# Kernel tuning notes

Measured on AMD Instinct MI355X. Metric: run time of the kernel, lower is better.

## Reference

```python
import jax, jax.numpy as jnp
import numpy as np

N, E, IN_DIM, H, D = 40000, 640000, 128, 8, 16


def setup_inputs() -> dict:
    key = jax.random.key(0)
    k_h, k_s, k_d, k_q, k_k, k_v = jax.random.split(key, 6)
    scale = float(np.sqrt(2.0 / (IN_DIM + H * D)))  # xavier-ish
    return {
        "h": jax.random.normal(k_h, (N, IN_DIM), dtype=jnp.float32),
        "src": jax.random.randint(k_s, (E,), 0, N, dtype=jnp.int32),
        "dst": jax.random.randint(k_d, (E,), 0, N, dtype=jnp.int32),
        "WQ": jax.random.normal(k_q, (IN_DIM, H * D), dtype=jnp.float32) * scale,
        "WK": jax.random.normal(k_k, (IN_DIM, H * D), dtype=jnp.float32) * scale,
        "WV": jax.random.normal(k_v, (IN_DIM, H * D), dtype=jnp.float32) * scale,
    }


def reference(h, src, dst, WQ, WK, WV):
    n = h.shape[0]
    Q = (h @ WQ).reshape(n, H, D)  # [N,H,D]
    K = (h @ WK).reshape(n, H, D)
    V = (h @ WV).reshape(n, H, D)
    inv_sqrt_d = 1.0 / jnp.sqrt(jnp.asarray(D, dtype=h.dtype))
    # per-edge elementwise score (DGL u_mul_v keeps the H x D vector)
    score = K[src] * Q[dst] * inv_sqrt_d  # [E,H,D]
    wV = jax.ops.segment_sum(V[src] * score, dst, num_segments=n)  # [N,H,D]
    z = jax.ops.segment_sum(score, dst, num_segments=n)            # [N,H,D]
    return wV / (z + 1e-6)
```

## Files before the change

kernel.cpp:

```cpp
#include <hip/hip_runtime.h>


#define FMA4(acc, s, b) do { \
    (acc).x = fmaf((s), (b).x, (acc).x); \
    (acc).y = fmaf((s), (b).y, (acc).y); \
    (acc).z = fmaf((s), (b).z, (acc).z); \
    (acc).w = fmaf((s), (b).w, (acc).w); } while (0)

__global__ __launch_bounds__(256) void gemm_qkv(
    const float* __restrict__ h,
    const float* __restrict__ WQ,
    const float* __restrict__ WK,
    const float* __restrict__ WV,
    float* __restrict__ Qf,
    float* __restrict__ KV,
    int N)
{
    __shared__ float4 Wl[32 * 32];
    __shared__ float4 Hl[128 * 8];
    const int t = threadIdx.x;
    const int which = blockIdx.y;
    const float* Wsel = (which == 0) ? WQ : ((which == 1) ? WK : WV);
    const float4* W4 = (const float4*)Wsel;
    const int r0 = blockIdx.x * 128;

    const int tc = t & 15;
    const int tr = t >> 4;

    float4 acc[8][2];
#pragma unroll
    for (int i = 0; i < 8; ++i) {
        acc[i][0] = make_float4(0.f, 0.f, 0.f, 0.f);
        acc[i][1] = make_float4(0.f, 0.f, 0.f, 0.f);
    }

    for (int kc = 0; kc < 4; ++kc) {
        __syncthreads();
#pragma unroll
        for (int i = 0; i < 4; ++i) {
            const int idx = t + i * 256;
            const int k = idx >> 5, c = idx & 31;
            Wl[idx] = W4[(size_t)(kc * 32 + k) * 32 + c];
        }
#pragma unroll
        for (int i = 0; i < 4; ++i) {
            const int idx = t + i * 256;
            const int row = idx >> 3, kk = idx & 7;
            float4 v = make_float4(0.f, 0.f, 0.f, 0.f);
            if (r0 + row < N)
                v = ((const float4*)h)[(size_t)(r0 + row) * 32 + kc * 8 + kk];
            Hl[row * 8 + kk] = v;
        }
        __syncthreads();

        for (int k4 = 0; k4 < 8; ++k4) {
            const float4 b0a = Wl[(k4 * 4 + 0) * 32 + tc * 2];
            const float4 b0b = Wl[(k4 * 4 + 0) * 32 + tc * 2 + 1];
            const float4 b1a = Wl[(k4 * 4 + 1) * 32 + tc * 2];
            const float4 b1b = Wl[(k4 * 4 + 1) * 32 + tc * 2 + 1];
            const float4 b2a = Wl[(k4 * 4 + 2) * 32 + tc * 2];
            const float4 b2b = Wl[(k4 * 4 + 2) * 32 + tc * 2 + 1];
            const float4 b3a = Wl[(k4 * 4 + 3) * 32 + tc * 2];
            const float4 b3b = Wl[(k4 * 4 + 3) * 32 + tc * 2 + 1];
#pragma unroll
            for (int r = 0; r < 8; ++r) {
                const float4 a = Hl[(tr * 8 + r) * 8 + k4];
                FMA4(acc[r][0], a.x, b0a); FMA4(acc[r][1], a.x, b0b);
                FMA4(acc[r][0], a.y, b1a); FMA4(acc[r][1], a.y, b1b);
                FMA4(acc[r][0], a.z, b2a); FMA4(acc[r][1], a.z, b2b);
                FMA4(acc[r][0], a.w, b3a); FMA4(acc[r][1], a.w, b3b);
            }
        }
    }

    float4* Obase = (which == 0) ? (float4*)Qf : (float4*)KV;
    const int ostride = (which == 0) ? 32 : 64;
    const int ooff = (which == 2) ? 32 : 0;
#pragma unroll
    for (int r = 0; r < 8; ++r) {
        const int row = r0 + tr * 8 + r;
        if (row < N) {
            Obase[(size_t)row * ostride + ooff + tc * 2]     = acc[r][0];
            Obase[(size_t)row * ostride + ooff + tc * 2 + 1] = acc[r][1];
        }
    }
}

__global__ __launch_bounds__(256) void count_deg(
    const int* __restrict__ dst, int* __restrict__ deg, int E)
{
    const int e = blockIdx.x * 256 + threadIdx.x;
    if (e < E) atomicAdd(&deg[dst[e]], 1);
}

__global__ __launch_bounds__(256) void chunk_reduce(
    const int* __restrict__ deg, int* __restrict__ csum, int N)
{
    const int t = threadIdx.x;
    const int i = blockIdx.x * 256 + t;
    int x = (i < N) ? deg[i] : 0;
#pragma unroll
    for (int off = 32; off; off >>= 1) x += __shfl_down(x, off, 64);
    __shared__ int ws[4];
    if ((t & 63) == 0) ws[t >> 6] = x;
    __syncthreads();
    if (t == 0) csum[blockIdx.x] = ws[0] + ws[1] + ws[2] + ws[3];
}

__global__ __launch_bounds__(256) void scan_chunks(
    const int* __restrict__ csum, int* __restrict__ coff, int nChunks)
{
    __shared__ int s[256];
    __shared__ int carry;
    const int t = threadIdx.x;
    if (t == 0) carry = 0;
    __syncthreads();
    for (int base = 0; base < nChunks; base += 256) {
        const int i = base + t;
        int x = (i < nChunks) ? csum[i] : 0;
        s[t] = x;
        __syncthreads();
        for (int off = 1; off < 256; off <<= 1) {
            int v = (t >= off) ? s[t - off] : 0;
            __syncthreads();
            s[t] += v;
            __syncthreads();
        }
        if (i < nChunks) coff[i] = carry + s[t] - x;
        __syncthreads();
        if (t == 0) carry += s[255];
        __syncthreads();
    }
}

__global__ __launch_bounds__(256) void chunk_scan(
    const int* __restrict__ deg, const int* __restrict__ coff,
    int* __restrict__ rowptr, int N)
{
    __shared__ int s[256];
    const int t = threadIdx.x;
    const int i = blockIdx.x * 256 + t;
    int x = (i < N) ? deg[i] : 0;
    s[t] = x;
    __syncthreads();
    for (int off = 1; off < 256; off <<= 1) {
        int v = (t >= off) ? s[t - off] : 0;
        __syncthreads();
        s[t] += v;
        __syncthreads();
    }
    if (i < N) rowptr[i + 1] = coff[blockIdx.x] + s[t];
    if (i == 0) rowptr[0] = 0;
}

__global__ __launch_bounds__(256) void scatter_pairs(
    const int* __restrict__ dst, const int* __restrict__ src,
    const int* __restrict__ rowptr, int* __restrict__ cur,
    int2* __restrict__ pairs, int E)
{
    const int e = blockIdx.x * 256 + threadIdx.x;
    if (e >= E) return;
    const int d = dst[e];
    const int pos = rowptr[d] + atomicAdd(&cur[d], 1);
    pairs[pos] = make_int2(e, src[e]);
}

__global__ __launch_bounds__(256) void rank_emit(
    const int* __restrict__ rowptr, const int2* __restrict__ pairs,
    int* __restrict__ srcs, int N)
{
    const int wave = threadIdx.x >> 6;
    const int lane = threadIdx.x & 63;
    const int d = blockIdx.x * 4 + wave;
    if (d >= N) return;
    const int lo = rowptr[d];
    const int deg = rowptr[d + 1] - lo;
    if (deg <= 64) {
        int2 p = make_int2(0x7fffffff, 0);
        if (lane < deg) p = pairs[lo + lane];
        int rank = 0;
        for (int j = 0; j < deg; ++j) {
            const int kj = __shfl(p.x, j, 64);
            rank += (kj < p.x) ? 1 : 0;
        }
        if (lane < deg) srcs[lo + rank] = p.y;
    } else if (lane == 0) {
        for (int i = 0; i < deg; ++i) {
            const int2 pi = pairs[lo + i];
            int rank = 0;
            for (int j = 0; j < deg; ++j) rank += (pairs[lo + j].x < pi.x) ? 1 : 0;
            srcs[lo + rank] = pi.y;
        }
    }
}

__global__ __launch_bounds__(128) void attn_out(
    const int* __restrict__ srcs, const int* __restrict__ rowptr,
    const float* __restrict__ KV, const float* __restrict__ Qf,
    float* __restrict__ out, int N)
{
#pragma clang fp contract(off)
    const int wave = threadIdx.x >> 6;
    const int lane = threadIdx.x & 63;
    const int d = blockIdx.x * 2 + wave;
    if (d >= N) return;
    const float2 q = ((const float2*)Qf)[(size_t)d * 64 + lane];
    const int lo = rowptr[d], hi = rowptr[d + 1];
    const float2* KV2 = (const float2*)KV;
    float2 z = make_float2(0.f, 0.f), wv = z;

#define EDGE_UPD(k, v) do { \
        float sc0 = ((k).x * q.x) * 0.25f; z.x = z.x + sc0; wv.x = wv.x + (v).x * sc0; \
        float sc1 = ((k).y * q.y) * 0.25f; z.y = z.y + sc1; wv.y = wv.y + (v).y * sc1; \
    } while (0)

    int i = lo;
    for (; i + 8 <= hi; i += 8) {
        int s[8];
#pragma unroll
        for (int u = 0; u < 8; ++u) s[u] = srcs[i + u];
        float2 kk[8], vv[8];
#pragma unroll
        for (int u = 0; u < 8; ++u) {
            kk[u] = KV2[(size_t)s[u] * 128 + lane];
            vv[u] = KV2[(size_t)s[u] * 128 + 64 + lane];
        }
#pragma unroll
        for (int u = 0; u < 8; ++u) EDGE_UPD(kk[u], vv[u]);
    }
    for (; i + 4 <= hi; i += 4) {
        const int s0 = srcs[i + 0], s1 = srcs[i + 1];
        const int s2 = srcs[i + 2], s3 = srcs[i + 3];
        const float2 k0 = KV2[(size_t)s0 * 128 + lane], v0 = KV2[(size_t)s0 * 128 + 64 + lane];
        const float2 k1 = KV2[(size_t)s1 * 128 + lane], v1 = KV2[(size_t)s1 * 128 + 64 + lane];
        const float2 k2 = KV2[(size_t)s2 * 128 + lane], v2 = KV2[(size_t)s2 * 128 + 64 + lane];
        const float2 k3 = KV2[(size_t)s3 * 128 + lane], v3 = KV2[(size_t)s3 * 128 + 64 + lane];
        EDGE_UPD(k0, v0); EDGE_UPD(k1, v1); EDGE_UPD(k2, v2); EDGE_UPD(k3, v3);
    }
    for (; i < hi; ++i) {
        const int s = srcs[i];
        const float2 k = KV2[(size_t)s * 128 + lane], v = KV2[(size_t)s * 128 + 64 + lane];
        EDGE_UPD(k, v);
    }
#undef EDGE_UPD

    float2 o;
    o.x = wv.x / (z.x + 1e-6f);
    o.y = wv.y / (z.y + 1e-6f);
    ((float2*)out)[(size_t)d * 64 + lane] = o;
}

extern "C" void kernel_launch(void* const* d_in, const int* in_sizes, int n_in,
                              void* d_out, int out_size, void* d_ws, size_t ws_size,
                              hipStream_t stream)
{
    const float* h  = (const float*)d_in[0];
    const int* src  = (const int*)d_in[1];
    const int* dst  = (const int*)d_in[2];
    const float* WQ = (const float*)d_in[3];
    const float* WK = (const float*)d_in[4];
    const float* WV = (const float*)d_in[5];
    const int N = in_sizes[0] / 128;
    const int E = in_sizes[1];
    const size_t NC = (size_t)N * 128;
    const int nChunks = (N + 255) / 256;

    float* KV = (float*)d_ws;
    float* Qf = KV + (size_t)N * 256;
    int* deg    = (int*)(Qf + NC);
    int* cur    = deg + N;
    int* rowptr = cur + N;
    int* csum   = rowptr + (N + 2);
    int* coff   = csum + nChunks;
    int* srcs   = coff + nChunks;
    int2* pairs = (int2*)(srcs + E);
    float* outp = (float*)d_out;

    hipMemsetAsync(deg, 0, (size_t)2 * N * sizeof(int), stream);

    dim3 ggrid((N + 127) / 128, 3);
    gemm_qkv<<<ggrid, 256, 0, stream>>>(h, WQ, WK, WV, Qf, KV, N);

    const int eb = (E + 255) / 256;
    count_deg<<<eb, 256, 0, stream>>>(dst, deg, E);
    chunk_reduce<<<nChunks, 256, 0, stream>>>(deg, csum, N);
    scan_chunks<<<1, 256, 0, stream>>>(csum, coff, nChunks);
    chunk_scan<<<nChunks, 256, 0, stream>>>(deg, coff, rowptr, N);
    scatter_pairs<<<eb, 256, 0, stream>>>(dst, src, rowptr, cur, pairs, E);
    rank_emit<<<(N + 3) / 4, 256, 0, stream>>>(rowptr, pairs, srcs, N);

    attn_out<<<(N + 1) / 2, 128, 0, stream>>>(srcs, rowptr, KV, Qf, outp, N);
}
```

Baseline: 302.1 us.

## Swizzle GEMM LDS, scatter edge ids only, prefetch next source indices

The QKV GEMM now stores h tiles in LDS with an XOR swizzle and spreads each thread's output columns as tc and tc+16, aiming to cut LDS bank conflicts. The CSR build scatters plain edge ids instead of (edge, src) pairs, halving that scatter's traffic, and looks up src[e] during the rank step. The attention kernel software-pipelines its 8-edge loop so the next batch of source indices loads while the current K/V gathers are consumed. This adds a dependent random read of src in rank_emit and more register pressure in attn_out.

```diff
diff --git a/kernel.cpp b/kernel.cpp
--- a/kernel.cpp
+++ b/kernel.cpp
@@ -49,22 +49,23 @@
             float4 v = make_float4(0.f, 0.f, 0.f, 0.f);
             if (r0 + row < N)
                 v = ((const float4*)h)[(size_t)(r0 + row) * 32 + kc * 8 + kk];
-            Hl[row * 8 + kk] = v;
+            Hl[row * 8 + (kk ^ ((row >> 3) & 7))] = v;
         }
         __syncthreads();
 
         for (int k4 = 0; k4 < 8; ++k4) {
-            const float4 b0a = Wl[(k4 * 4 + 0) * 32 + tc * 2];
-            const float4 b0b = Wl[(k4 * 4 + 0) * 32 + tc * 2 + 1];
-            const float4 b1a = Wl[(k4 * 4 + 1) * 32 + tc * 2];
-            const float4 b1b = Wl[(k4 * 4 + 1) * 32 + tc * 2 + 1];
-            const float4 b2a = Wl[(k4 * 4 + 2) * 32 + tc * 2];
-            const float4 b2b = Wl[(k4 * 4 + 2) * 32 + tc * 2 + 1];
-            const float4 b3a = Wl[(k4 * 4 + 3) * 32 + tc * 2];
-            const float4 b3b = Wl[(k4 * 4 + 3) * 32 + tc * 2 + 1];
+            const float4 b0a = Wl[(k4 * 4 + 0) * 32 + tc];
+            const float4 b0b = Wl[(k4 * 4 + 0) * 32 + tc + 16];
+            const float4 b1a = Wl[(k4 * 4 + 1) * 32 + tc];
+            const float4 b1b = Wl[(k4 * 4 + 1) * 32 + tc + 16];
+            const float4 b2a = Wl[(k4 * 4 + 2) * 32 + tc];
+            const float4 b2b = Wl[(k4 * 4 + 2) * 32 + tc + 16];
+            const float4 b3a = Wl[(k4 * 4 + 3) * 32 + tc];
+            const float4 b3b = Wl[(k4 * 4 + 3) * 32 + tc + 16];
 #pragma unroll
             for (int r = 0; r < 8; ++r) {
-                const float4 a = Hl[(tr * 8 + r) * 8 + k4];
+                const int row = tr * 8 + r;
+                const float4 a = Hl[row * 8 + (k4 ^ (tr & 7))];
                 FMA4(acc[r][0], a.x, b0a); FMA4(acc[r][1], a.x, b0b);
                 FMA4(acc[r][0], a.y, b1a); FMA4(acc[r][1], a.y, b1b);
                 FMA4(acc[r][0], a.z, b2a); FMA4(acc[r][1], a.z, b2b);
@@ -80,8 +81,8 @@
     for (int r = 0; r < 8; ++r) {
         const int row = r0 + tr * 8 + r;
         if (row < N) {
-            Obase[(size_t)row * ostride + ooff + tc * 2]     = acc[r][0];
-            Obase[(size_t)row * ostride + ooff + tc * 2 + 1] = acc[r][1];
+            Obase[(size_t)row * ostride + ooff + tc]      = acc[r][0];
+            Obase[(size_t)row * ostride + ooff + tc + 16] = acc[r][1];
         }
     }
 }
@@ -153,21 +154,20 @@
     if (i == 0) rowptr[0] = 0;
 }
 
-__global__ __launch_bounds__(256) void scatter_pairs(
-    const int* __restrict__ dst, const int* __restrict__ src,
-    const int* __restrict__ rowptr, int* __restrict__ cur,
-    int2* __restrict__ pairs, int E)
+__global__ __launch_bounds__(256) void scatter_eids(
+    const int* __restrict__ dst, const int* __restrict__ rowptr,
+    int* __restrict__ cur, int* __restrict__ eids, int E)
 {
     const int e = blockIdx.x * 256 + threadIdx.x;
     if (e >= E) return;
     const int d = dst[e];
     const int pos = rowptr[d] + atomicAdd(&cur[d], 1);
-    pairs[pos] = make_int2(e, src[e]);
+    eids[pos] = e;
 }
 
 __global__ __launch_bounds__(256) void rank_emit(
-    const int* __restrict__ rowptr, const int2* __restrict__ pairs,
-    int* __restrict__ srcs, int N)
+    const int* __restrict__ rowptr, const int* __restrict__ eids,
+    const int* __restrict__ src, int* __restrict__ srcs, int N)
 {
     const int wave = threadIdx.x >> 6;
     const int lane = threadIdx.x & 63;
@@ -176,20 +176,20 @@
     const int lo = rowptr[d];
     const int deg = rowptr[d + 1] - lo;
     if (deg <= 64) {
-        int2 p = make_int2(0x7fffffff, 0);
-        if (lane < deg) p = pairs[lo + lane];
+        int p = 0x7fffffff;
+        if (lane < deg) p = eids[lo + lane];
         int rank = 0;
         for (int j = 0; j < deg; ++j) {
-            const int kj = __shfl(p.x, j, 64);
-            rank += (kj < p.x) ? 1 : 0;
-        }
-        if (lane < deg) srcs[lo + rank] = p.y;
+            const int kj = __shfl(p, j, 64);
+            rank += (kj < p) ? 1 : 0;
+        }
+        if (lane < deg) srcs[lo + rank] = src[p];
     } else if (lane == 0) {
         for (int i = 0; i < deg; ++i) {
-            const int2 pi = pairs[lo + i];
+            const int pi = eids[lo + i];
             int rank = 0;
-            for (int j = 0; j < deg; ++j) rank += (pairs[lo + j].x < pi.x) ? 1 : 0;
-            srcs[lo + rank] = pi.y;
+            for (int j = 0; j < deg; ++j) rank += (eids[lo + j] < pi) ? 1 : 0;
+            srcs[lo + rank] = src[pi];
         }
     }
 }
@@ -215,31 +215,47 @@
     } while (0)
 
     int i = lo;
-    for (; i + 8 <= hi; i += 8) {
-        int s[8];
+    int s[8];
+    bool have = (i + 8 <= hi);
+    if (have) {
 #pragma unroll
         for (int u = 0; u < 8; ++u) s[u] = srcs[i + u];
+    }
+    while (have) {
         float2 kk[8], vv[8];
 #pragma unroll
         for (int u = 0; u < 8; ++u) {
             kk[u] = KV2[(size_t)s[u] * 128 + lane];
             vv[u] = KV2[(size_t)s[u] * 128 + 64 + lane];
         }
+        const int i2 = i + 8;
+        const bool have2 = (i2 + 8 <= hi);
+        int s2[8];
+        if (have2) {
+#pragma unroll
+            for (int u = 0; u < 8; ++u) s2[u] = srcs[i2 + u];
+        }
 #pragma unroll
         for (int u = 0; u < 8; ++u) EDGE_UPD(kk[u], vv[u]);
+        i = i2;
+        have = have2;
+        if (have2) {
+#pragma unroll
+            for (int u = 0; u < 8; ++u) s[u] = s2[u];
+        }
     }
     for (; i + 4 <= hi; i += 4) {
         const int s0 = srcs[i + 0], s1 = srcs[i + 1];
-        const int s2 = srcs[i + 2], s3 = srcs[i + 3];
+        const int s2b = srcs[i + 2], s3 = srcs[i + 3];
         const float2 k0 = KV2[(size_t)s0 * 128 + lane], v0 = KV2[(size_t)s0 * 128 + 64 + lane];
         const float2 k1 = KV2[(size_t)s1 * 128 + lane], v1 = KV2[(size_t)s1 * 128 + 64 + lane];
-        const float2 k2 = KV2[(size_t)s2 * 128 + lane], v2 = KV2[(size_t)s2 * 128 + 64 + lane];
+        const float2 k2 = KV2[(size_t)s2b * 128 + lane], v2 = KV2[(size_t)s2b * 128 + 64 + lane];
         const float2 k3 = KV2[(size_t)s3 * 128 + lane], v3 = KV2[(size_t)s3 * 128 + 64 + lane];
         EDGE_UPD(k0, v0); EDGE_UPD(k1, v1); EDGE_UPD(k2, v2); EDGE_UPD(k3, v3);
     }
     for (; i < hi; ++i) {
-        const int s = srcs[i];
-        const float2 k = KV2[(size_t)s * 128 + lane], v = KV2[(size_t)s * 128 + 64 + lane];
+        const int sx = srcs[i];
+        const float2 k = KV2[(size_t)sx * 128 + lane], v = KV2[(size_t)sx * 128 + 64 + lane];
         EDGE_UPD(k, v);
     }
 #undef EDGE_UPD
@@ -270,10 +286,10 @@
     int* deg    = (int*)(Qf + NC);
     int* cur    = deg + N;
     int* rowptr = cur + N;
-    int* csum   = rowptr + (N + 2);
+    int* csum   = rowptr + (N + 1);
     int* coff   = csum + nChunks;
     int* srcs   = coff + nChunks;
-    int2* pairs = (int2*)(srcs + E);
+    int* eids   = srcs + E;
     float* outp = (float*)d_out;
 
     hipMemsetAsync(deg, 0, (size_t)2 * N * sizeof(int), stream);
@@ -286,8 +302,8 @@
     chunk_reduce<<<nChunks, 256, 0, stream>>>(deg, csum, N);
     scan_chunks<<<1, 256, 0, stream>>>(csum, coff, nChunks);
     chunk_scan<<<nChunks, 256, 0, stream>>>(deg, coff, rowptr, N);
-    scatter_pairs<<<eb, 256, 0, stream>>>(dst, src, rowptr, cur, pairs, E);
-    rank_emit<<<(N + 3) / 4, 256, 0, stream>>>(rowptr, pairs, srcs, N);
+    scatter_eids<<<eb, 256, 0, stream>>>(dst, rowptr, cur, eids, E);
+    rank_emit<<<(N + 3) / 4, 256, 0, stream>>>(rowptr, eids, src, srcs, N);
 
     attn_out<<<(N + 1) / 2, 128, 0, stream>>>(srcs, rowptr, KV, Qf, outp, N);
 }
```

Measured after the change: 294.8 us. 2.4% less time.
